# Performance work log

Measured on AMD Instinct MI355X. Metric: run time of the kernel, lower is better.

Reference implementation:

```python
import jax, jax.numpy as jnp
import numpy as np

B, N, L, C, K, NL, FF = 8, 2048, 2048, 256, 16, 2, 4
RADIUS = 0.12


def setup_inputs() -> dict:
    key = jax.random.key(0)
    ks = jax.random.split(key, 18)
    s = 0.02
    return {
        "q_xyz": jax.random.uniform(ks[0], (B, N, 3), dtype=jnp.float32),
        "q_feat": jax.random.normal(ks[1], (B, N, C), dtype=jnp.float32),
        "kv_xyz": jax.random.uniform(ks[2], (B, L, 3), dtype=jnp.float32),
        "kv_feat": jax.random.normal(ks[3], (B, L, C), dtype=jnp.float32),
        # PointTransformerConv linears (bias=False in PyG)
        "W_src": jax.random.normal(ks[4], (NL, C, C), dtype=jnp.float32) * s,
        "W_dst": jax.random.normal(ks[5], (NL, C, C), dtype=jnp.float32) * s,
        "W_lin": jax.random.normal(ks[6], (NL, C, C), dtype=jnp.float32) * s,
        # attn_nn = Linear(C,C)+ReLU (MLP plain_last=False)
        "W_attn": jax.random.normal(ks[7], (NL, C, C), dtype=jnp.float32) * s,
        "b_attn": jnp.zeros((NL, C), dtype=jnp.float32),
        # FFN
        "W1": jax.random.normal(ks[8], (NL, C, C * FF), dtype=jnp.float32) * s,
        "b1": jnp.zeros((NL, C * FF), dtype=jnp.float32),
        "W2": jax.random.normal(ks[9], (NL, C * FF, C), dtype=jnp.float32) * s,
        "b2": jnp.zeros((NL, C), dtype=jnp.float32),
        # LayerNorms
        "ln1_g": jnp.ones((NL, C), dtype=jnp.float32),
        "ln1_b": jnp.zeros((NL, C), dtype=jnp.float32),
        "ln2_g": jnp.ones((NL, C), dtype=jnp.float32),
        "ln2_b": jnp.zeros((NL, C), dtype=jnp.float32),
    }


def _ln(x, g, b, eps=1e-5):
    mu = x.mean(-1, keepdims=True)
    var = ((x - mu) ** 2).mean(-1, keepdims=True)
    return (x - mu) * jax.lax.rsqrt(var + eps) * g + b


def reference(q_xyz, q_feat, kv_xyz, kv_feat, W_src, W_dst, W_lin, W_attn,
              b_attn, W1, b1, W2, b2, ln1_g, ln1_b, ln2_g, ln2_b):
    # radius ball query: up to K nearest kv points within RADIUS of each query
    d2 = jnp.sum((q_xyz[:, :, None, :] - kv_xyz[:, None, :, :]) ** 2, axis=-1)  # [B,N,L]
    neg, idx = jax.lax.top_k(-d2, K)            # idx: [B,N,K] into L
    valid = (-neg) <= RADIUS * RADIUS           # [B,N,K] in-ball mask
    vmask = valid[..., None].astype(q_feat.dtype)

    gather = jax.vmap(lambda a, i: a[i])        # [B,L,C],[B,N,K] -> [B,N,K,C]
    out = q_feat
    for i in range(NL):
        a_src = kv_feat @ W_src[i]              # [B,L,C]
        a_dst = out @ W_dst[i]                  # [B,N,C]
        v = kv_feat @ W_lin[i]                  # [B,L,C]
        a_src_g = gather(a_src, idx)            # [B,N,K,C]
        v_g = gather(v, idx)                    # [B,N,K,C]
        # attn_nn(lin_dst(x_i) - lin_src(x_j) + delta), delta=0 (ZeroPos)
        alpha = jax.nn.relu(
            jnp.einsum('bnkc,cd->bnkd', a_dst[:, :, None, :] - a_src_g, W_attn[i]) + b_attn[i])
        logits = jnp.where(valid[..., None], alpha, -1e9)
        attn = jax.nn.softmax(logits, axis=2) * vmask   # per-channel softmax over neighbors
        conv = jnp.sum(attn * v_g, axis=2)              # [B,N,C]
        out = _ln(out + conv, ln1_g[i], ln1_b[i])
        h = jax.nn.gelu(out @ W1[i] + b1[i], approximate=False)
        out = _ln(out + h @ W2[i] + b2[i], ln2_g[i], ln2_b[i])
    return out
```

## Files before the change

### kernel.cpp

```cpp
#include <hip/hip_runtime.h>
#include <math.h>

#define BB 8
#define NN 2048
#define LL 2048
#define CC 256
#define KK 16
#define NL 2
#define FF 4

typedef __attribute__((ext_vector_type(8))) short short8v;
typedef __attribute__((ext_vector_type(4))) float f32x4;

__device__ __forceinline__ short f2b(float f) {
    unsigned u = __float_as_uint(f);
    u += 0x7FFFu + ((u >> 16) & 1u);
    return (short)(u >> 16);
}
__device__ __forceinline__ float b2f(short s) {
    return __uint_as_float(((unsigned)(unsigned short)s) << 16);
}
__device__ __forceinline__ float blo(unsigned u) {
    return __uint_as_float(u << 16);
}
__device__ __forceinline__ float bhi(unsigned u) {
    return __uint_as_float(u & 0xffff0000u);
}

__global__ __launch_bounds__(256) void init_k(const float* __restrict__ src,
                                              float* __restrict__ dst,
                                              short* __restrict__ dstb) {
    size_t i = ((size_t)blockIdx.x * 256 + threadIdx.x) * 4;
    float4 v = *reinterpret_cast<const float4*>(src + i);
    *reinterpret_cast<float4*>(dst + i) = v;
    short o[4] = {f2b(v.x), f2b(v.y), f2b(v.z), f2b(v.w)};
    *reinterpret_cast<int2*>(dstb + i) = *reinterpret_cast<int2*>(o);
}

__global__ __launch_bounds__(256) void f2b_k(const float* __restrict__ in,
                                             short* __restrict__ out) {
    size_t i = ((size_t)blockIdx.x * 256 + threadIdx.x) * 4;
    float4 v = *reinterpret_cast<const float4*>(in + i);
    short o[4] = {f2b(v.x), f2b(v.y), f2b(v.z), f2b(v.w)};
    *reinterpret_cast<int2*>(out + i) = *reinterpret_cast<int2*>(o);
}

__global__ __launch_bounds__(256) void tconvB_k(const float* __restrict__ W0,
                                                short* __restrict__ Wt0,
                                                int K, int N,
                                                size_t sin, size_t sout) {
    const float* W = W0 + (size_t)blockIdx.z * sin;
    short* Wt = Wt0 + (size_t)blockIdx.z * sout;
    __shared__ float tile[32][33];
    const int n0 = blockIdx.x * 32, k0 = blockIdx.y * 32;
    const int tx = threadIdx.x & 31, ty = threadIdx.x >> 5;
#pragma unroll
    for (int r = 0; r < 32; r += 8)
        tile[ty + r][tx] = W[(size_t)(k0 + ty + r) * N + n0 + tx];
    __syncthreads();
#pragma unroll
    for (int r = 0; r < 32; r += 8)
        Wt[(size_t)(n0 + ty + r) * K + k0 + tx] = f2b(tile[tx][ty + r]);
}

#define QPB 32
#define CAP 48
__global__ __launch_bounds__(256) void knn_k(const float* __restrict__ qxyz,
                                             const float* __restrict__ kvxyz,
                                             int* __restrict__ idx,
                                             float* __restrict__ valid) {
    __shared__ float4 sxyz[LL];
    __shared__ unsigned long long cpk[QPB][CAP + 1];
    __shared__ int ccnt[QPB];

    const int t   = threadIdx.x;
    const int q   = t >> 3;
    const int sub = t & 7;
    const int b   = blockIdx.x >> 6;
    const int n   = ((blockIdx.x & 63) << 5) + q;

    const float* kb = kvxyz + (size_t)b * LL * 3;
    for (int p = t; p < LL; p += 256)
        sxyz[p] = make_float4(kb[3 * p], kb[3 * p + 1], kb[3 * p + 2], 0.f);
    if (t < QPB) ccnt[t] = 0;
    __syncthreads();

    const size_t qo = (size_t)(b * NN + n) * 3;
    const float qx = qxyz[qo], qy = qxyz[qo + 1], qz = qxyz[qo + 2];
    const float rad2 = (float)(0.12 * 0.12);

    for (int j = sub; j < LL; j += 32) {
        float4 p0 = sxyz[j];
        float4 p1 = sxyz[j + 8];
        float4 p2 = sxyz[j + 16];
        float4 p3 = sxyz[j + 24];
        float x0 = qx - p0.x, y0 = qy - p0.y, z0 = qz - p0.z;
        float x1 = qx - p1.x, y1 = qy - p1.y, z1 = qz - p1.z;
        float x2 = qx - p2.x, y2 = qy - p2.y, z2 = qz - p2.z;
        float x3 = qx - p3.x, y3 = qy - p3.y, z3 = qz - p3.z;
        float d0 = fmaf(x0, x0, fmaf(y0, y0, z0 * z0));
        float d1 = fmaf(x1, x1, fmaf(y1, y1, z1 * z1));
        float d2 = fmaf(x2, x2, fmaf(y2, y2, z2 * z2));
        float d3 = fmaf(x3, x3, fmaf(y3, y3, z3 * z3));
        if (fminf(fminf(d0, d1), fminf(d2, d3)) <= rad2) {
            if (d0 <= rad2) {
                int s = atomicAdd(&ccnt[q], 1);
                if (s < CAP) cpk[q][s] = ((unsigned long long)__float_as_uint(d0) << 32) | (unsigned)(j);
            }
            if (d1 <= rad2) {
                int s = atomicAdd(&ccnt[q], 1);
                if (s < CAP) cpk[q][s] = ((unsigned long long)__float_as_uint(d1) << 32) | (unsigned)(j + 8);
            }
            if (d2 <= rad2) {
                int s = atomicAdd(&ccnt[q], 1);
                if (s < CAP) cpk[q][s] = ((unsigned long long)__float_as_uint(d2) << 32) | (unsigned)(j + 16);
            }
            if (d3 <= rad2) {
                int s = atomicAdd(&ccnt[q], 1);
                if (s < CAP) cpk[q][s] = ((unsigned long long)__float_as_uint(d3) << 32) | (unsigned)(j + 24);
            }
        }
    }
    __syncthreads();

    int c = ccnt[q]; if (c > CAP) c = CAP;
    const size_t o = (size_t)(b * NN + n) * KK;
#pragma unroll 1
    for (int j = sub; j < c; j += 8) {
        const unsigned long long v = cpk[q][j];
        int rank = 0;
#pragma unroll 1
        for (int i = 0; i < c; ++i) rank += (cpk[q][i] < v) ? 1 : 0;
        if (rank < KK) {
            idx[o + rank]   = (int)(v & 0xffffffffu);
            valid[o + rank] = 1.0f;
        }
    }
#pragma unroll
    for (int k = sub; k < KK; k += 8)
        if (k >= c) { idx[o + k] = 0; valid[o + k] = 0.0f; }
}

template <int ACT, int OBF>
__device__ __forceinline__ void mm_body(const short* __restrict__ A,
                                        const short* __restrict__ Bt,
                                        const float* __restrict__ bias,
                                        void* __restrict__ Cout,
                                        int M, int N, int Kd) {
    __shared__ __align__(16) short As[128 * 32];
    __shared__ __align__(16) short Bs[128 * 32];
    const int t = threadIdx.x;
    const int lane = t & 63;
    const int wv = t >> 6;
    const int wr = wv >> 1, wc = wv & 1;
    const int lrow = lane & 15;
    const int kc = lane >> 4;
    const int row0 = blockIdx.y * 128;
    const int col0 = blockIdx.x * 128;

    f32x4 acc[4][4];
#pragma unroll
    for (int m = 0; m < 4; ++m)
#pragma unroll
        for (int n = 0; n < 4; ++n) acc[m][n] = f32x4{0.f, 0.f, 0.f, 0.f};

    const int r0 = t >> 2, cch = t & 3;
    const int r1 = r0 + 64;

    for (int k0 = 0; k0 < Kd; k0 += 32) {
        __syncthreads();
        {
            int4 va = *(const int4*)(A  + (size_t)(row0 + r0) * Kd + k0 + cch * 8);
            int4 vb = *(const int4*)(Bt + (size_t)(col0 + r0) * Kd + k0 + cch * 8);
            *(int4*)(As + r0 * 32 + ((cch ^ ((r0 >> 1) & 3)) * 8)) = va;
            *(int4*)(Bs + r0 * 32 + ((cch ^ ((r0 >> 1) & 3)) * 8)) = vb;
            int4 va2 = *(const int4*)(A  + (size_t)(row0 + r1) * Kd + k0 + cch * 8);
            int4 vb2 = *(const int4*)(Bt + (size_t)(col0 + r1) * Kd + k0 + cch * 8);
            *(int4*)(As + r1 * 32 + ((cch ^ ((r1 >> 1) & 3)) * 8)) = va2;
            *(int4*)(Bs + r1 * 32 + ((cch ^ ((r1 >> 1) & 3)) * 8)) = vb2;
        }
        __syncthreads();
        short8v af[4], bf[4];
#pragma unroll
        for (int m = 0; m < 4; ++m) {
            const int ar = wr * 64 + m * 16 + lrow;
            af[m] = *(const short8v*)(As + ar * 32 + ((kc ^ ((ar >> 1) & 3)) * 8));
        }
#pragma unroll
        for (int n = 0; n < 4; ++n) {
            const int br = wc * 64 + n * 16 + lrow;
            bf[n] = *(const short8v*)(Bs + br * 32 + ((kc ^ ((br >> 1) & 3)) * 8));
        }
#pragma unroll
        for (int m = 0; m < 4; ++m)
#pragma unroll
            for (int n = 0; n < 4; ++n)
                acc[m][n] = __builtin_amdgcn_mfma_f32_16x16x32_bf16(
                    af[m], bf[n], acc[m][n], 0, 0, 0);
    }

    float bcol[4];
#pragma unroll
    for (int n = 0; n < 4; ++n)
        bcol[n] = bias ? bias[col0 + wc * 64 + n * 16 + lrow] : 0.f;

#pragma unroll
    for (int m = 0; m < 4; ++m) {
#pragma unroll
        for (int n = 0; n < 4; ++n) {
            const int col = col0 + wc * 64 + n * 16 + lrow;
#pragma unroll
            for (int r = 0; r < 4; ++r) {
                const int row = row0 + wr * 64 + m * 16 + kc * 4 + r;
                float v = acc[m][n][r] + bcol[n];
                if (ACT == 1) v = 0.5f * v * (1.0f + erff(v * 0.70710678118654752f));
                if (OBF) ((short*)Cout)[(size_t)row * N + col] = f2b(v);
                else     ((float*)Cout)[(size_t)row * N + col] = v;
            }
        }
    }
}

template <int ACT, int OBF>
__global__ __launch_bounds__(256) void mm_k(const short* __restrict__ A,
                                            const short* __restrict__ Bt,
                                            const float* __restrict__ bias,
                                            void* __restrict__ Cout,
                                            int M, int N, int Kd) {
    mm_body<ACT, OBF>(A, Bt, bias, Cout, M, N, Kd);
}

__global__ __launch_bounds__(256) void wcomb_k(const short* __restrict__ WatT,
                                               const short* __restrict__ Wdst16,
                                               const short* __restrict__ Wsrc16,
                                               short* __restrict__ WcdT,
                                               short* __restrict__ Wsv) {
    const int z = blockIdx.z, i = z >> 1, sel = z & 1;
    const short* A = WatT + (size_t)i * CC * CC;
    const short* B = (sel ? Wsrc16 : Wdst16) + (size_t)i * CC * CC;
    short* C = sel ? (Wsv + (size_t)i * 2 * CC * CC) : (WcdT + (size_t)i * CC * CC);
    mm_body<0, 1>(A, B, nullptr, C, CC, CC, CC);
}

#define AQB 4
__global__ __launch_bounds__(256) void attn_ln_k(
    const short* __restrict__ dw, const short* __restrict__ swv,
    const int* __restrict__ idx, const float* __restrict__ valid,
    const float* __restrict__ bat,
    const float* __restrict__ ln_g, const float* __restrict__ ln_b,
    float* __restrict__ out, short* __restrict__ outb) {
    __shared__ int   sidx[AQB * KK];
    __shared__ float sval[AQB * KK];
    __shared__ __align__(16) float sconv[AQB][CC];
    const int t = threadIdx.x;
    const int b   = blockIdx.x & 7;
    const int blk = blockIdx.x >> 3;
    const int bn0 = b * NN + blk * AQB;
    const size_t boff = (size_t)b * LL;

    if (t < AQB * KK) {
        sidx[t] = idx[(size_t)bn0 * KK + t];
        sval[t] = valid[(size_t)bn0 * KK + t];
    }
    __syncthreads();

    const int cp = (t & 127) * 2;
    const int qh = t >> 7;
    const float bias0 = bat[cp], bias1 = bat[cp + 1];
    const unsigned* swvu = (const unsigned*)swv;

#pragma unroll
    for (int qq = 0; qq < 2; ++qq) {
        const int q = qh * 2 + qq;
        const int bn = bn0 + q;
        const unsigned du = *(const unsigned*)(dw + (size_t)bn * CC + cp);
        const float d0 = blo(du) + bias0;
        const float d1 = bhi(du) + bias1;
        float s0 = 0.f, s1 = 0.f, n0 = 0.f, n1 = 0.f;
#pragma unroll
        for (int k = 0; k < KK; ++k) {
            const int j = sidx[q * KK + k];
            const float vv = sval[q * KK + k];
            const unsigned* rp = swvu + (boff + j) * CC;
            const unsigned su = rp[cp >> 1];
            const unsigned vu = rp[128 + (cp >> 1)];
            const float e0 = vv * __expf(fmaxf(d0 - blo(su), 0.f));
            const float e1 = vv * __expf(fmaxf(d1 - bhi(su), 0.f));
            s0 += e0; s1 += e1;
            n0 = fmaf(e0, blo(vu), n0);
            n1 = fmaf(e1, bhi(vu), n1);
        }
        sconv[q][cp]     = (s0 > 0.f) ? n0 / s0 : 0.f;
        sconv[q][cp + 1] = (s1 > 0.f) ? n1 / s1 : 0.f;
    }
    __syncthreads();

    const int lane = t & 63, w = t >> 6;
    float4 gg = *reinterpret_cast<const float4*>(&ln_g[lane * 4]);
    float4 bb = *reinterpret_cast<const float4*>(&ln_b[lane * 4]);
    {
        const int q = w;
        const size_t base = (size_t)(bn0 + q) * CC + lane * 4;
        float4 x = *reinterpret_cast<const float4*>(&out[base]);
        float4 d = *reinterpret_cast<const float4*>(&sconv[q][lane * 4]);
        float v0 = x.x + d.x, v1 = x.y + d.y, v2 = x.z + d.z, v3 = x.w + d.w;
        float s = v0 + v1 + v2 + v3;
#pragma unroll
        for (int o = 32; o > 0; o >>= 1) s += __shfl_xor(s, o);
        const float mu = s * (1.0f / 256.0f);
        const float t0 = v0 - mu, t1 = v1 - mu, t2 = v2 - mu, t3 = v3 - mu;
        float qv = t0 * t0 + t1 * t1 + t2 * t2 + t3 * t3;
#pragma unroll
        for (int o = 32; o > 0; o >>= 1) qv += __shfl_xor(qv, o);
        const float rstd = rsqrtf(qv * (1.0f / 256.0f) + 1e-5f);
        float4 y;
        y.x = t0 * rstd * gg.x + bb.x;
        y.y = t1 * rstd * gg.y + bb.y;
        y.z = t2 * rstd * gg.z + bb.z;
        y.w = t3 * rstd * gg.w + bb.w;
        *reinterpret_cast<float4*>(&out[base]) = y;
        short o4[4] = {f2b(y.x), f2b(y.y), f2b(y.z), f2b(y.w)};
        *reinterpret_cast<int2*>(outb + base) = *reinterpret_cast<int2*>(o4);
    }
}

__global__ __launch_bounds__(256) void add_ln_k(float* __restrict__ out,
                                                const float* __restrict__ del,
                                                const float* __restrict__ g,
                                                const float* __restrict__ bt,
                                                short* __restrict__ ob) {
    const int row  = blockIdx.x * 4 + (threadIdx.x >> 6);
    const int lane = threadIdx.x & 63;
    const size_t base = (size_t)row * CC + lane * 4;
    float4 x = *reinterpret_cast<const float4*>(&out[base]);
    float4 d = *reinterpret_cast<const float4*>(&del[base]);
    float v0 = x.x + d.x, v1 = x.y + d.y, v2 = x.z + d.z, v3 = x.w + d.w;

    float s = v0 + v1 + v2 + v3;
#pragma unroll
    for (int o = 32; o > 0; o >>= 1) s += __shfl_xor(s, o);
    const float mu = s * (1.0f / 256.0f);
    const float t0 = v0 - mu, t1 = v1 - mu, t2 = v2 - mu, t3 = v3 - mu;
    float q = t0 * t0 + t1 * t1 + t2 * t2 + t3 * t3;
#pragma unroll
    for (int o = 32; o > 0; o >>= 1) q += __shfl_xor(q, o);
    const float rstd = rsqrtf(q * (1.0f / 256.0f) + 1e-5f);

    float4 gg = *reinterpret_cast<const float4*>(&g[lane * 4]);
    float4 bb = *reinterpret_cast<const float4*>(&bt[lane * 4]);
    float4 y;
    y.x = t0 * rstd * gg.x + bb.x;
    y.y = t1 * rstd * gg.y + bb.y;
    y.z = t2 * rstd * gg.z + bb.z;
    y.w = t3 * rstd * gg.w + bb.w;
    *reinterpret_cast<float4*>(&out[base]) = y;
    short o4[4] = {f2b(y.x), f2b(y.y), f2b(y.z), f2b(y.w)};
    *reinterpret_cast<int2*>(ob + base) = *reinterpret_cast<int2*>(o4);
}

extern "C" void kernel_launch(void* const* d_in, const int* in_sizes, int n_in,
                              void* d_out, int out_size, void* d_ws, size_t ws_size,
                              hipStream_t stream) {
    const float* q_xyz   = (const float*)d_in[0];
    const float* q_feat  = (const float*)d_in[1];
    const float* kv_xyz  = (const float*)d_in[2];
    const float* kv_feat = (const float*)d_in[3];
    const float* W_src   = (const float*)d_in[4];
    const float* W_dst   = (const float*)d_in[5];
    const float* W_lin   = (const float*)d_in[6];
    const float* W_attn  = (const float*)d_in[7];
    const float* b_attn  = (const float*)d_in[8];
    const float* W1      = (const float*)d_in[9];
    const float* b1      = (const float*)d_in[10];
    const float* W2      = (const float*)d_in[11];
    const float* b2      = (const float*)d_in[12];
    const float* ln1_g   = (const float*)d_in[13];
    const float* ln1_b   = (const float*)d_in[14];
    const float* ln2_g   = (const float*)d_in[15];
    const float* ln2_b   = (const float*)d_in[16];

    float* out = (float*)d_out;
    char* wsb = (char*)d_ws;
    const size_t MB = (size_t)1 << 20;
    int*   idxb   = (int*)(wsb);
    float* validb = (float*)(wsb + 1 * MB);
    short* kvf16  = (short*)(wsb + 2 * MB);
    short* outb16 = (short*)(wsb + 10 * MB);
    short* dw16   = (short*)(wsb + 18 * MB);
    short* swv16  = (short*)(wsb + 26 * MB);
    short* h16    = (short*)(wsb + 42 * MB);
    float* convb  = (float*)(wsb + 74 * MB);
    short* WatT   = (short*)(wsb + 90 * MB);
    short* Wdst16 = (short*)(wsb + 90 * MB + 256 * 1024);
    short* Wsrc16 = (short*)(wsb + 90 * MB + 512 * 1024);
    short* WcdT   = (short*)(wsb + 90 * MB + 768 * 1024);
    short* Wsv    = (short*)(wsb + 91 * MB);
    short* W1T    = (short*)(wsb + 92 * MB);
    short* W2T    = (short*)(wsb + 93 * MB);

    const int M = BB * NN;

    init_k<<<M * CC / (256 * 4), 256, 0, stream>>>(q_feat, out, outb16);
    f2b_k<<<M * CC / (256 * 4), 256, 0, stream>>>(kv_feat, kvf16);
    f2b_k<<<NL * CC * CC / (256 * 4), 256, 0, stream>>>(W_dst, Wdst16);
    f2b_k<<<NL * CC * CC / (256 * 4), 256, 0, stream>>>(W_src, Wsrc16);
    knn_k<<<BB * (NN / QPB), 256, 0, stream>>>(q_xyz, kv_xyz, idxb, validb);

    tconvB_k<<<dim3(8, 8, NL), 256, 0, stream>>>(W_attn, WatT, CC, CC,
                                                 (size_t)CC * CC, (size_t)CC * CC);
    tconvB_k<<<dim3(8, 8, NL), 256, 0, stream>>>(W_lin, Wsv + CC * CC, CC, CC,
                                                 (size_t)CC * CC, (size_t)2 * CC * CC);
    tconvB_k<<<dim3(32, 8, NL), 256, 0, stream>>>(W1, W1T, CC, CC * FF,
                                                  (size_t)CC * CC * FF, (size_t)CC * CC * FF);
    tconvB_k<<<dim3(8, 32, NL), 256, 0, stream>>>(W2, W2T, CC * FF, CC,
                                                  (size_t)CC * CC * FF, (size_t)CC * CC * FF);
    wcomb_k<<<dim3(2, 2, 2 * NL), 256, 0, stream>>>(WatT, Wdst16, Wsrc16, WcdT, Wsv);

    for (int i = 0; i < NL; ++i) {
        const size_t oC = (size_t)i * CC * CC;
        const size_t oF = (size_t)i * CC * CC * FF;
        const float* bat = b_attn + (size_t)i * CC;
        const float* b1p = b1 + (size_t)i * CC * FF;
        const float* b2p = b2 + (size_t)i * CC;

        mm_k<0, 1><<<dim3(2, 128), 256, 0, stream>>>(outb16, WcdT + oC, nullptr, dw16, M, CC, CC);
        mm_k<0, 1><<<dim3(4, 128), 256, 0, stream>>>(kvf16, Wsv + (size_t)i * 2 * CC * CC,
                                                     nullptr, swv16, M, 2 * CC, CC);

        attn_ln_k<<<M / AQB, 256, 0, stream>>>(dw16, swv16, idxb, validb, bat,
                                               ln1_g + (size_t)i * CC, ln1_b + (size_t)i * CC,
                                               out, outb16);

        mm_k<1, 1><<<dim3(8, 128), 256, 0, stream>>>(outb16, W1T + oF, b1p, h16, M, CC * FF, CC);
        mm_k<0, 0><<<dim3(2, 128), 256, 0, stream>>>(h16, W2T + oF, b2p, convb, M, CC, CC * FF);
        add_ln_k<<<M / 4, 256, 0, stream>>>(out, convb,
                                            ln2_g + (size_t)i * CC, ln2_b + (size_t)i * CC, outb16);
    }
    (void)in_sizes; (void)n_in; (void)out_size; (void)ws_size;
}
```

Before: 288.4 us.

## Use direct global-to-LDS loads in GEMM and merge projection GEMM launches

The bf16 GEMM tile loader now uses the global_load_lds builtin to copy 16-byte chunks straight from global memory into shared memory, instead of staging them through registers. The XOR swizzle moves from the store side to the load address, so the shared-memory layout stays the same. Shared buffers are now passed into mm_body from the caller, which lets a new mmpair_k kernel run the dst projection GEMM and the src/value projection GEMM in a single launch by splitting the block range. The goal is to cut register pressure and load-issue overhead and to remove one launch per layer, at the cost of relying on the compiler to insert correct vmcnt waits for the asynchronous LDS writes.

```diff
diff --git a/kernel.cpp b/kernel.cpp
--- a/kernel.cpp
+++ b/kernel.cpp
@@ -25,6 +25,12 @@
 }
 __device__ __forceinline__ float bhi(unsigned u) {
     return __uint_as_float(u & 0xffff0000u);
+}
+
+__device__ __forceinline__ void g2l16(const void* g, void* l) {
+    __builtin_amdgcn_global_load_lds(
+        (const __attribute__((address_space(1))) void*)g,
+        (__attribute__((address_space(3))) void*)l, 16, 0, 0);
 }
 
 __global__ __launch_bounds__(256) void init_k(const float* __restrict__ src,
@@ -142,21 +148,20 @@
 }
 
 template <int ACT, int OBF>
-__device__ __forceinline__ void mm_body(const short* __restrict__ A,
+__device__ __forceinline__ void mm_body(short* As, short* Bs,
+                                        const short* __restrict__ A,
                                         const short* __restrict__ Bt,
                                         const float* __restrict__ bias,
                                         void* __restrict__ Cout,
-                                        int M, int N, int Kd) {
-    __shared__ __align__(16) short As[128 * 32];
-    __shared__ __align__(16) short Bs[128 * 32];
+                                        int N, int Kd, int bx, int by) {
     const int t = threadIdx.x;
     const int lane = t & 63;
     const int wv = t >> 6;
     const int wr = wv >> 1, wc = wv & 1;
     const int lrow = lane & 15;
     const int kc = lane >> 4;
-    const int row0 = blockIdx.y * 128;
-    const int col0 = blockIdx.x * 128;
+    const int row0 = by * 128;
+    const int col0 = bx * 128;
 
     f32x4 acc[4][4];
 #pragma unroll
@@ -165,20 +170,14 @@
         for (int n = 0; n < 4; ++n) acc[m][n] = f32x4{0.f, 0.f, 0.f, 0.f};
 
     const int r0 = t >> 2, cch = t & 3;
-    const int r1 = r0 + 64;
+    const int scch = cch ^ ((r0 >> 1) & 3);
 
     for (int k0 = 0; k0 < Kd; k0 += 32) {
         __syncthreads();
-        {
-            int4 va = *(const int4*)(A  + (size_t)(row0 + r0) * Kd + k0 + cch * 8);
-            int4 vb = *(const int4*)(Bt + (size_t)(col0 + r0) * Kd + k0 + cch * 8);
-            *(int4*)(As + r0 * 32 + ((cch ^ ((r0 >> 1) & 3)) * 8)) = va;
-            *(int4*)(Bs + r0 * 32 + ((cch ^ ((r0 >> 1) & 3)) * 8)) = vb;
-            int4 va2 = *(const int4*)(A  + (size_t)(row0 + r1) * Kd + k0 + cch * 8);
-            int4 vb2 = *(const int4*)(Bt + (size_t)(col0 + r1) * Kd + k0 + cch * 8);
-            *(int4*)(As + r1 * 32 + ((cch ^ ((r1 >> 1) & 3)) * 8)) = va2;
-            *(int4*)(Bs + r1 * 32 + ((cch ^ ((r1 >> 1) & 3)) * 8)) = vb2;
-        }
+        g2l16(A  + (size_t)(row0 + r0) * Kd + k0 + scch * 8,       As + t * 8);
+        g2l16(A  + (size_t)(row0 + r0 + 64) * Kd + k0 + scch * 8,  As + 2048 + t * 8);
+        g2l16(Bt + (size_t)(col0 + r0) * Kd + k0 + scch * 8,       Bs + t * 8);
+        g2l16(Bt + (size_t)(col0 + r0 + 64) * Kd + k0 + scch * 8,  Bs + 2048 + t * 8);
         __syncthreads();
         short8v af[4], bf[4];
 #pragma unroll
@@ -227,7 +226,22 @@
                                             const float* __restrict__ bias,
                                             void* __restrict__ Cout,
                                             int M, int N, int Kd) {
-    mm_body<ACT, OBF>(A, Bt, bias, Cout, M, N, Kd);
+    __shared__ __align__(16) short As[128 * 32];
+    __shared__ __align__(16) short Bs[128 * 32];
+    mm_body<ACT, OBF>(As, Bs, A, Bt, bias, Cout, N, Kd, blockIdx.x, blockIdx.y);
+    (void)M;
+}
+
+__global__ __launch_bounds__(256) void mmpair_k(
+    const short* A0, const short* Bt0, void* C0, int N0,
+    const short* A1, const short* Bt1, void* C1, int N1, int Kd) {
+    __shared__ __align__(16) short As[128 * 32];
+    __shared__ __align__(16) short Bs[128 * 32];
+    const int nb0 = N0 >> 7;
+    if ((int)blockIdx.x < nb0)
+        mm_body<0, 1>(As, Bs, A0, Bt0, nullptr, C0, N0, Kd, blockIdx.x, blockIdx.y);
+    else
+        mm_body<0, 1>(As, Bs, A1, Bt1, nullptr, C1, N1, Kd, blockIdx.x - nb0, blockIdx.y);
 }
 
 __global__ __launch_bounds__(256) void wcomb_k(const short* __restrict__ WatT,
@@ -235,11 +249,13 @@
                                                const short* __restrict__ Wsrc16,
                                                short* __restrict__ WcdT,
                                                short* __restrict__ Wsv) {
+    __shared__ __align__(16) short As[128 * 32];
+    __shared__ __align__(16) short Bs[128 * 32];
     const int z = blockIdx.z, i = z >> 1, sel = z & 1;
     const short* A = WatT + (size_t)i * CC * CC;
     const short* B = (sel ? Wsrc16 : Wdst16) + (size_t)i * CC * CC;
     short* C = sel ? (Wsv + (size_t)i * 2 * CC * CC) : (WcdT + (size_t)i * CC * CC);
-    mm_body<0, 1>(A, B, nullptr, C, CC, CC, CC);
+    mm_body<0, 1>(As, Bs, A, B, nullptr, C, CC, CC, blockIdx.x, blockIdx.y);
 }
 
 #define AQB 4
@@ -417,15 +433,15 @@
     wcomb_k<<<dim3(2, 2, 2 * NL), 256, 0, stream>>>(WatT, Wdst16, Wsrc16, WcdT, Wsv);
 
     for (int i = 0; i < NL; ++i) {
+        const size_t oF = (size_t)i * CC * CC * FF;
         const size_t oC = (size_t)i * CC * CC;
-        const size_t oF = (size_t)i * CC * CC * FF;
         const float* bat = b_attn + (size_t)i * CC;
         const float* b1p = b1 + (size_t)i * CC * FF;
         const float* b2p = b2 + (size_t)i * CC;
 
-        mm_k<0, 1><<<dim3(2, 128), 256, 0, stream>>>(outb16, WcdT + oC, nullptr, dw16, M, CC, CC);
-        mm_k<0, 1><<<dim3(4, 128), 256, 0, stream>>>(kvf16, Wsv + (size_t)i * 2 * CC * CC,
-                                                     nullptr, swv16, M, 2 * CC, CC);
+        mmpair_k<<<dim3(6, 128), 256, 0, stream>>>(
+            outb16, WcdT + oC, dw16, CC,
+            kvf16, Wsv + (size_t)i * 2 * CC * CC, swv16, 2 * CC, CC);
 
         attn_ln_k<<<M / AQB, 256, 0, stream>>>(dw16, swv16, idxb, validb, bat,
                                                ln1_g + (size_t)i * CC, ln1_b + (size_t)i * CC,
```

Result: no change. 283.8 us (-1.6%).
